# Performance work log

Hardware: AMD Instinct MI355X
Metric: run time of the kernel (lower is better)

The kernel has to match this reference:

```python
import jax, jax.numpy as jnp
import numpy as np

B, S, D = 8, 2048, 256


def setup_inputs() -> dict:
    key = jax.random.key(0)
    ks = jax.random.split(key, 8)
    nodes = jax.random.normal(ks[0], (B, S, D), dtype=jnp.float32)
    mask = jax.random.randint(ks[1], (B, S), 0, 2, dtype=jnp.int32)
    # ensure at least one unmasked position per row to avoid all--inf softmax
    mask = mask.at[:, 0].set(1)
    scale = 1.0 / np.sqrt(D)
    Wq = jax.random.normal(ks[2], (D, D), dtype=jnp.float32) * scale
    bq = jnp.zeros((D,), dtype=jnp.float32)
    Wk = jax.random.normal(ks[3], (D, D), dtype=jnp.float32) * scale
    bk = jnp.zeros((D,), dtype=jnp.float32)
    Wv = jax.random.normal(ks[4], (D, D), dtype=jnp.float32) * scale
    bv = jnp.zeros((D,), dtype=jnp.float32)
    return {"nodes": nodes, "mask": mask, "Wq": Wq, "bq": bq,
            "Wk": Wk, "bk": bk, "Wv": Wv, "bv": bv}


def reference(nodes, mask, Wq, bq, Wk, bk, Wv, bv):
    # Linear layers: x @ W.T + b (torch nn.Linear convention)
    q = jnp.einsum('bsd,ed->bse', nodes, Wq) + bq   # [B,S,D]
    k = jnp.einsum('bsd,ed->bse', nodes, Wk) + bk
    v = jnp.einsum('bsd,ed->bse', nodes, Wv) + bv
    d = k.shape[-1]
    scores = jnp.einsum('bqd,bkd->bqk', q, k) / jnp.sqrt(jnp.float32(d))  # [B,S,S]
    # mask[b, j] == 0 masks key column j for every query row
    scores = jnp.where(mask[:, None, :] != 0, scores, -jnp.inf)
    attn = jax.nn.softmax(scores, axis=-1)           # [B,S,S]
    weighted = jnp.einsum('bqk,bkd->bqd', attn, v)   # [B,S,D]
    return jnp.mean(weighted, axis=1)                # [B,D]
```

## Files before the change

### kernel.cpp

```cpp
#include <hip/hip_runtime.h>
#include <hip/hip_bf16.h>
#include <stdint.h>


typedef short short8 __attribute__((ext_vector_type(8)));
typedef float floatx4 __attribute__((ext_vector_type(4)));
typedef float floatx2 __attribute__((ext_vector_type(2)));

#define MFMA16(a, b, c) __builtin_amdgcn_mfma_f32_16x16x32_bf16((a), (b), (c), 0, 0, 0)

#define ASYNC16(gsrc, ldst)                                                    \
    __builtin_amdgcn_global_load_lds(                                          \
        (__attribute__((address_space(1))) void*)(void*)(gsrc),                \
        (__attribute__((address_space(3))) void*)(ldst), 16, 0, 0)

static __device__ __forceinline__ unsigned short f2bf(float f) {
    union { float f; unsigned u; } v; v.f = f;
    unsigned r = v.u + 0x7fffu + ((v.u >> 16) & 1u);
    return (unsigned short)(r >> 16);
}
static __device__ __forceinline__ float bf2f(unsigned short h) {
    union { unsigned u; float f; } v; v.u = ((unsigned)h) << 16;
    return v.f;
}

__global__ __launch_bounds__(256) void k_cc(
    const float* __restrict__ nodes, const float* __restrict__ Wq,
    const float* __restrict__ Wk, const float* __restrict__ Wv,
    unsigned short* __restrict__ nbf, unsigned short* __restrict__ wbf,
    const int* __restrict__ mask, int* __restrict__ cidx, int* __restrict__ cnt,
    float* __restrict__ zbase ,
    float* __restrict__ outp )
{
    int blk = blockIdx.x;
    if (blk < 2144) {
        int unit = blk * 256 + threadIdx.x;
        const float* src;
        unsigned short* dst;
        int off;
        if (unit < 524288) {
            src = nodes; dst = nbf; off = unit * 8;
        } else {
            int j = (unit - 524288) * 8;
            int m = j >> 16;
            int r = j & 65535;
            src = (m == 0) ? Wq : (m == 1 ? Wk : Wv);
            dst = wbf + m * 65536;
            off = r;
        }
        float4 a = *(const float4*)(src + off);
        float4 b = *(const float4*)(src + off + 4);
        short8 o;
        o[0] = f2bf(a.x); o[1] = f2bf(a.y); o[2] = f2bf(a.z); o[3] = f2bf(a.w);
        o[4] = f2bf(b.x); o[5] = f2bf(b.y); o[6] = f2bf(b.z); o[7] = f2bf(b.w);
        *(short8*)(dst + off) = o;
        return;
    }
    if (blk < 2152) {
        if (threadIdx.x < 64) {
            int b = blk - 2144, lane = threadIdx.x;
            int base = 0;
            for (int c = 0; c < 2048; c += 64) {
                int m = mask[b * 2048 + c + lane];
                unsigned long long bal = __ballot(m != 0);
                int pre = __popcll(bal & ((1ull << lane) - 1ull));
                if (m) cidx[b * 2048 + base + pre] = c + lane;
                base += __popcll(bal);
            }
            if (lane == 0) cnt[b] = base;
            for (int i = base + lane; i < 2048; i += 64) cidx[b * 2048 + i] = 0;
        }
        return;
    }
    int idx = (blk - 2152) * 256 + threadIdx.x;
    float4 z = {0.f, 0.f, 0.f, 0.f};
#pragma unroll
    for (int j = 0; j < 2; ++j) {
        int p = idx + j * 4352;
        if (p < 8192) ((float4*)zbase)[p] = z;
        else ((float4*)outp)[p - 8192] = z;
    }
}

__global__ __launch_bounds__(256) void k_proj2a(
    const unsigned short* __restrict__ nbf,
    const unsigned short* __restrict__ wbf,
    const float* __restrict__ bq, const float* __restrict__ bk,
    const float* __restrict__ bv,
    unsigned short* __restrict__ qb, unsigned short* __restrict__ kb,
    unsigned short* __restrict__ vb)
{
    __shared__ __align__(16) unsigned short As[128 * 64];
    __shared__ __align__(16) unsigned short Bs[128 * 64];
    int tid = threadIdx.x, lane = tid & 63, wave = tid >> 6;
    int wm = wave & 1, wn = wave >> 1;
    int l15 = lane & 15, quad = lane >> 4;
    int mBase = blockIdx.x * 128;
    int nBase = blockIdx.y * 128;
    int z = blockIdx.z;
    const unsigned short* W = wbf + z * 65536;

    floatx4 acc[4][4] = {};

    for (int kc = 0; kc < 256; kc += 64) {
#pragma unroll
        for (int i = 0; i < 4; ++i) {
            int p = i * 256 + wave * 64 + lane;
            int row = p >> 3;
            int col8 = (p & 7) ^ (row & 7);
            int goff = row * 256 + kc + col8 * 8;
            unsigned short* dstA = &As[(i * 256 + wave * 64) * 8];
            unsigned short* dstB = &Bs[(i * 256 + wave * 64) * 8];
            ASYNC16(nbf + mBase * 256 + goff, dstA);
            ASYNC16(W + nBase * 256 + goff, dstB);
        }
        __syncthreads();
#pragma unroll
        for (int ks = 0; ks < 2; ++ks) {
            int c8 = ks * 4 + quad;
            short8 af[4], bfr[4];
#pragma unroll
            for (int i = 0; i < 4; ++i) {
                int row = wm * 64 + i * 16 + l15;
                af[i] = *(const short8*)(&As[(row * 8 + (c8 ^ (row & 7))) * 8]);
            }
#pragma unroll
            for (int i = 0; i < 4; ++i) {
                int row = wn * 64 + i * 16 + l15;
                bfr[i] = *(const short8*)(&Bs[(row * 8 + (c8 ^ (row & 7))) * 8]);
            }
#pragma unroll
            for (int mi = 0; mi < 4; ++mi)
#pragma unroll
                for (int ni = 0; ni < 4; ++ni)
                    acc[mi][ni] = MFMA16(af[mi], bfr[ni], acc[mi][ni]);
        }
        __syncthreads();
    }

    const float* bias = (z == 0) ? bq : (z == 1 ? bk : bv);
    unsigned short* out = (z == 0) ? qb : (z == 1 ? kb : vb);
    float scale = (z == 0) ? 0.0625f : 1.0f;
#pragma unroll
    for (int mi = 0; mi < 4; ++mi)
#pragma unroll
        for (int ni = 0; ni < 4; ++ni) {
            int col = nBase + wn * 64 + ni * 16 + l15;
            float bval = bias[col];
#pragma unroll
            for (int r = 0; r < 4; ++r) {
                int row = mBase + wm * 64 + mi * 16 + quad * 4 + r;
                out[row * 256 + col] = f2bf((acc[mi][ni][r] + bval) * scale);
            }
        }
}

__global__ __launch_bounds__(256) void k_repack(
    const unsigned short* __restrict__ kb, const int* __restrict__ cidx,
    const int* __restrict__ cnt_g, unsigned short* __restrict__ kbt)
{
    int c = blockIdx.x, b = blockIdx.y;
    int cnt = cnt_g[b];
    if (c * 64 >= cnt) return;
    size_t obase = ((size_t)b * 32 + c) * 16384;
#pragma unroll
    for (int i = 0; i < 8; ++i) {
        int idx = i * 256 + threadIdx.x;
        int du = idx >> 6, key = idx & 63;
        int krow = cidx[b * 2048 + c * 64 + key];
        short8 v = *(const short8*)(kb + ((size_t)b * 2048 + krow) * 256 + du * 8);
        *(short8*)(kbt + obase + (size_t)idx * 8) = v;
    }
}

__global__ __launch_bounds__(256) void k_pass1v(
    const unsigned short* __restrict__ qb, const unsigned short* __restrict__ kbt,
    const int* __restrict__ cnt_g, float* __restrict__ lsum_g,
    unsigned char* __restrict__ pbuf)
{
    __shared__ __align__(16) unsigned short kt[16384];
    int tid = threadIdx.x, lane = tid & 63, wave = tid >> 6;
    int l15 = lane & 15, quad = lane >> 4;
    int b = blockIdx.z;
    int cnt = cnt_g[b];
    int nchunk = (cnt + 63) >> 6;
    int qBase = blockIdx.x * 128 + wave * 32;
    int qcg = blockIdx.x * 4 + wave;

    short8 qf[2][8];
#pragma unroll
    for (int mi = 0; mi < 2; ++mi)
#pragma unroll
        for (int ks = 0; ks < 8; ++ks)
            qf[mi][ks] = *(const short8*)(qb + (b * 2048 + qBase + mi * 16 + l15) * 256 + ks * 32 + quad * 8);

    float ls[2][4] = {};
    for (int c = blockIdx.y; c < nchunk; c += 4) {
        const unsigned short* src = kbt + ((size_t)b * 32 + c) * 16384;
#pragma unroll
        for (int i = 0; i < 8; ++i) {
            int seg = wave * 8 + i;
            ASYNC16(src + seg * 512 + lane * 8, &kt[seg * 512]);
        }
        __syncthreads();
#pragma unroll
        for (int nt = 0; nt < 4; ++nt) {
            short8 kf[8];
#pragma unroll
            for (int ks = 0; ks < 8; ++ks)
                kf[ks] = *(const short8*)(&kt[((ks * 4 + quad) * 64 + nt * 16 + l15) * 8]);
            floatx4 acc[2] = {};
#pragma unroll
            for (int ks = 0; ks < 8; ++ks) {
                acc[0] = MFMA16(qf[0][ks], kf[ks], acc[0]);
                acc[1] = MFMA16(qf[1][ks], kf[ks], acc[1]);
            }
            float bias = (c * 64 + nt * 16 + l15 < cnt) ? 0.0f : -1e30f;
            float e[2][4];
#pragma unroll
            for (int mi = 0; mi < 2; ++mi)
#pragma unroll
                for (int r = 0; r < 4; ++r) {
                    e[mi][r] = __expf(acc[mi][r] + bias);
                    ls[mi][r] += e[mi][r];
                }
            int ktile = c * 4 + nt;
            if (ktile < 96) {
                int w0 = __builtin_amdgcn_cvt_pk_fp8_f32(e[0][0], e[0][1], 0, 0);
                w0 = __builtin_amdgcn_cvt_pk_fp8_f32(e[0][2], e[0][3], w0, 1);
                int w1 = __builtin_amdgcn_cvt_pk_fp8_f32(e[1][0], e[1][1], 0, 0);
                w1 = __builtin_amdgcn_cvt_pk_fp8_f32(e[1][2], e[1][3], w1, 1);
                size_t off = ((((size_t)b * 96 + ktile) * 64 + qcg) * 64 + lane) * 8;
                uint2 pv; pv.x = (unsigned)w0; pv.y = (unsigned)w1;
                *(uint2*)(pbuf + off) = pv;
            }
        }
        __syncthreads();
    }
#pragma unroll
    for (int mi = 0; mi < 2; ++mi)
#pragma unroll
        for (int r = 0; r < 4; ++r) {
            float v = ls[mi][r];
            v += __shfl_xor(v, 1); v += __shfl_xor(v, 2);
            v += __shfl_xor(v, 4); v += __shfl_xor(v, 8);
            if (l15 == 0)
                atomicAdd(&lsum_g[b * 2048 + qBase + mi * 16 + quad * 4 + r], v);
        }
}

__global__ __launch_bounds__(512) void k_wred5(
    const unsigned char* __restrict__ pbuf, const float* __restrict__ lsum_g,
    const int* __restrict__ cidx, const int* __restrict__ cnt_g,
    float* __restrict__ wsum_g)
{
    __shared__ float linv_p[2048];
    int tid = threadIdx.x, lane = tid & 63, wave = tid >> 6;
    int l15 = lane & 15, quad = lane >> 4;
    int b = blockIdx.z;
    int ktile = blockIdx.y * 8 + wave;

#pragma unroll
    for (int i = 0; i < 4; ++i) {
        int idx = i * 512 + tid;
        int qcg = idx >> 5, qd = (idx >> 3) & 3, j = idx & 7;
        int q = qcg * 32 + (j >> 2) * 16 + qd * 4 + (j & 3);
        linv_p[idx] = 1.0f / lsum_g[b * 2048 + q];
    }
    __syncthreads();

    int cnt = cnt_g[b];
    if (ktile >= 96 || ktile * 16 >= cnt) return;

    int qcg0 = blockIdx.x * 32;
    float acc = 0.f;
#pragma unroll 4
    for (int qcg = qcg0; qcg < qcg0 + 32; ++qcg) {
        size_t off = ((((size_t)b * 96 + ktile) * 64 + qcg) * 64 + lane) * 8;
        uint2 pv = *(const uint2*)(pbuf + off);
        const float* lv = &linv_p[(qcg * 4 + quad) * 8];
        floatx2 p01 = __builtin_amdgcn_cvt_pk_f32_fp8(pv.x, 0);
        floatx2 p23 = __builtin_amdgcn_cvt_pk_f32_fp8(pv.x, 1);
        floatx2 p45 = __builtin_amdgcn_cvt_pk_f32_fp8(pv.y, 0);
        floatx2 p67 = __builtin_amdgcn_cvt_pk_f32_fp8(pv.y, 1);
        acc += p01[0] * lv[0] + p01[1] * lv[1] + p23[0] * lv[2] + p23[1] * lv[3]
             + p45[0] * lv[4] + p45[1] * lv[5] + p67[0] * lv[6] + p67[1] * lv[7];
    }
    acc += __shfl_xor(acc, 16);
    acc += __shfl_xor(acc, 32);
    int slot = ktile * 16 + l15;
    if (lane < 16 && slot < cnt)
        atomicAdd(&wsum_g[b * 2048 + cidx[b * 2048 + slot]], acc);
}

__global__ __launch_bounds__(256) void k_out(
    const float* __restrict__ wsum_g, const unsigned short* __restrict__ vb,
    float* __restrict__ outp)
{
    int b = blockIdx.y;
    int d = threadIdx.x;
    int k0 = blockIdx.x * 128;
    float acc = 0.f;
#pragma unroll 4
    for (int k = k0; k < k0 + 128; ++k) {
        float wv = wsum_g[b * 2048 + k];
        acc += wv * bf2f(vb[(b * 2048 + k) * 256 + d]);
    }
    atomicAdd(&outp[b * 256 + d], acc * (1.0f / 2048.0f));
}

extern "C" void kernel_launch(void* const* d_in, const int* in_sizes, int n_in,
                              void* d_out, int out_size, void* d_ws, size_t ws_size,
                              hipStream_t stream)
{
    const float* nodes = (const float*)d_in[0];
    const int*   mask  = (const int*)d_in[1];
    const float* Wq    = (const float*)d_in[2];
    const float* bq    = (const float*)d_in[3];
    const float* Wk    = (const float*)d_in[4];
    const float* bk    = (const float*)d_in[5];
    const float* Wv    = (const float*)d_in[6];
    const float* bv    = (const float*)d_in[7];
    float* out = (float*)d_out;

    unsigned short* qb  = (unsigned short*)d_ws;
    unsigned short* kb  = qb + 4194304;
    unsigned short* vb  = kb + 4194304;
    float* lsum = (float*)(vb + 4194304);
    float* wsum = lsum + 16384;
    int*   cnt  = (int*)(wsum + 16384);
    int*   cidx = cnt + 16;
    unsigned short* kbt = (unsigned short*)(cidx + 16384);
    unsigned short* X   = kbt + 4194304;
    unsigned short* nbf = X;
    unsigned short* wbf = X + 4194304;
    unsigned char* pbuf = (unsigned char*)X;

    k_cc<<<2169, 256, 0, stream>>>(nodes, Wq, Wk, Wv, nbf, wbf,
                                   mask, cidx, cnt, lsum, out);
    k_proj2a<<<dim3(128, 2, 3), 256, 0, stream>>>(nbf, wbf, bq, bk, bv, qb, kb, vb);
    k_repack<<<dim3(32, 8), 256, 0, stream>>>(kb, cidx, cnt, kbt);
    k_pass1v<<<dim3(16, 4, 8), 256, 0, stream>>>(qb, kbt, cnt, lsum, pbuf);
    k_wred5<<<dim3(2, 16, 8), 512, 0, stream>>>(pbuf, lsum, cidx, cnt, wsum);
    k_out<<<dim3(16, 8), 256, 0, stream>>>(wsum, vb, out);
}
```

Baseline: 142.3 us.

## Fuse K repack into projection epilogue via slot map scatter

The mask-compaction step now also builds a per-row slot map and zero-fills the padded tail of the compacted K buffer. The projection kernel writes K directly into the compacted, transposed kbt layout using that map, so the separate repack kernel and the intermediate K buffer are removed. This saves one launch and a full read/write pass over K. In exchange, the K epilogue does scattered 2-byte stores with a per-row slot lookup, which may coalesce poorly.

```diff
diff --git a/kernel.cpp b/kernel.cpp
--- a/kernel.cpp
+++ b/kernel.cpp
@@ -29,6 +29,8 @@
     const float* __restrict__ Wk, const float* __restrict__ Wv,
     unsigned short* __restrict__ nbf, unsigned short* __restrict__ wbf,
     const int* __restrict__ mask, int* __restrict__ cidx, int* __restrict__ cnt,
+    int* __restrict__ slot_of ,
+    unsigned short* __restrict__ kbt,
     float* __restrict__ zbase ,
     float* __restrict__ outp )
 {
@@ -64,11 +66,26 @@
                 int m = mask[b * 2048 + c + lane];
                 unsigned long long bal = __ballot(m != 0);
                 int pre = __popcll(bal & ((1ull << lane) - 1ull));
-                if (m) cidx[b * 2048 + base + pre] = c + lane;
+                if (m) {
+                    cidx[b * 2048 + base + pre] = c + lane;
+                    slot_of[b * 2048 + c + lane] = base + pre;
+                } else {
+                    slot_of[b * 2048 + c + lane] = -1;
+                }
                 base += __popcll(bal);
             }
             if (lane == 0) cnt[b] = base;
             for (int i = base + lane; i < 2048; i += 64) cidx[b * 2048 + i] = 0;
+            int cntPad = (base + 63) & ~63;
+            int pad = cntPad - base;
+            short8 z8 = {};
+            for (int i = lane; i < pad * 32; i += 64) {
+                int slot = base + (i >> 5);
+                int du = i & 31;
+                size_t off = ((size_t)b * 32 + (slot >> 6)) * 16384
+                           + ((size_t)du * 64 + (slot & 63)) * 8;
+                *(short8*)(kbt + off) = z8;
+            }
         }
         return;
     }
@@ -82,12 +99,13 @@
     }
 }
 
-__global__ __launch_bounds__(256) void k_proj2a(
+__global__ __launch_bounds__(256) void k_proj2b(
     const unsigned short* __restrict__ nbf,
     const unsigned short* __restrict__ wbf,
     const float* __restrict__ bq, const float* __restrict__ bk,
     const float* __restrict__ bv,
-    unsigned short* __restrict__ qb, unsigned short* __restrict__ kb,
+    const int* __restrict__ slot_of,
+    unsigned short* __restrict__ qb, unsigned short* __restrict__ kbt,
     unsigned short* __restrict__ vb)
 {
     __shared__ __align__(16) unsigned short As[128 * 64];
@@ -139,37 +157,41 @@
     }
 
     const float* bias = (z == 0) ? bq : (z == 1 ? bk : bv);
-    unsigned short* out = (z == 0) ? qb : (z == 1 ? kb : vb);
     float scale = (z == 0) ? 0.0625f : 1.0f;
-#pragma unroll
-    for (int mi = 0; mi < 4; ++mi)
-#pragma unroll
-        for (int ni = 0; ni < 4; ++ni) {
-            int col = nBase + wn * 64 + ni * 16 + l15;
-            float bval = bias[col];
-#pragma unroll
-            for (int r = 0; r < 4; ++r) {
-                int row = mBase + wm * 64 + mi * 16 + quad * 4 + r;
-                out[row * 256 + col] = f2bf((acc[mi][ni][r] + bval) * scale);
-            }
-        }
-}
-
-__global__ __launch_bounds__(256) void k_repack(
-    const unsigned short* __restrict__ kb, const int* __restrict__ cidx,
-    const int* __restrict__ cnt_g, unsigned short* __restrict__ kbt)
-{
-    int c = blockIdx.x, b = blockIdx.y;
-    int cnt = cnt_g[b];
-    if (c * 64 >= cnt) return;
-    size_t obase = ((size_t)b * 32 + c) * 16384;
-#pragma unroll
-    for (int i = 0; i < 8; ++i) {
-        int idx = i * 256 + threadIdx.x;
-        int du = idx >> 6, key = idx & 63;
-        int krow = cidx[b * 2048 + c * 64 + key];
-        short8 v = *(const short8*)(kb + ((size_t)b * 2048 + krow) * 256 + du * 8);
-        *(short8*)(kbt + obase + (size_t)idx * 8) = v;
+    if (z == 1) {
+#pragma unroll
+        for (int mi = 0; mi < 4; ++mi)
+#pragma unroll
+            for (int ni = 0; ni < 4; ++ni) {
+                int col = nBase + wn * 64 + ni * 16 + l15;
+                float bval = bias[col];
+                int du = col >> 3, cj = col & 7;
+#pragma unroll
+                for (int r = 0; r < 4; ++r) {
+                    int row = mBase + wm * 64 + mi * 16 + quad * 4 + r;
+                    int slot = slot_of[row];
+                    if (slot >= 0) {
+                        int b = row >> 11;
+                        size_t off = ((size_t)b * 32 + (slot >> 6)) * 16384
+                                   + ((size_t)du * 64 + (slot & 63)) * 8 + cj;
+                        kbt[off] = f2bf(acc[mi][ni][r] + bval);
+                    }
+                }
+            }
+    } else {
+        unsigned short* out = (z == 0) ? qb : vb;
+#pragma unroll
+        for (int mi = 0; mi < 4; ++mi)
+#pragma unroll
+            for (int ni = 0; ni < 4; ++ni) {
+                int col = nBase + wn * 64 + ni * 16 + l15;
+                float bval = bias[col];
+#pragma unroll
+                for (int r = 0; r < 4; ++r) {
+                    int row = mBase + wm * 64 + mi * 16 + quad * 4 + r;
+                    out[row * 256 + col] = f2bf((acc[mi][ni][r] + bval) * scale);
+                }
+            }
     }
 }
 
@@ -324,22 +346,22 @@
     float* out = (float*)d_out;
 
     unsigned short* qb  = (unsigned short*)d_ws;
-    unsigned short* kb  = qb + 4194304;
-    unsigned short* vb  = kb + 4194304;
+    unsigned short* vb  = qb + 4194304;
     float* lsum = (float*)(vb + 4194304);
     float* wsum = lsum + 16384;
     int*   cnt  = (int*)(wsum + 16384);
     int*   cidx = cnt + 16;
-    unsigned short* kbt = (unsigned short*)(cidx + 16384);
+    int*   slot_of = cidx + 16384;
+    unsigned short* kbt = (unsigned short*)(slot_of + 16384);
     unsigned short* X   = kbt + 4194304;
     unsigned short* nbf = X;
     unsigned short* wbf = X + 4194304;
     unsigned char* pbuf = (unsigned char*)X;
 
     k_cc<<<2169, 256, 0, stream>>>(nodes, Wq, Wk, Wv, nbf, wbf,
-                                   mask, cidx, cnt, lsum, out);
-    k_proj2a<<<dim3(128, 2, 3), 256, 0, stream>>>(nbf, wbf, bq, bk, bv, qb, kb, vb);
-    k_repack<<<dim3(32, 8), 256, 0, stream>>>(kb, cidx, cnt, kbt);
+                                   mask, cidx, cnt, slot_of, kbt, lsum, out);
+    k_proj2b<<<dim3(128, 2, 3), 256, 0, stream>>>(nbf, wbf, bq, bk, bv,
+                                                  slot_of, qb, kbt, vb);
     k_pass1v<<<dim3(16, 4, 8), 256, 0, stream>>>(qb, kbt, cnt, lsum, pbuf);
     k_wred5<<<dim3(2, 16, 8), 512, 0, stream>>>(pbuf, lsum, cidx, cnt, wsum);
     k_out<<<dim3(16, 8), 256, 0, stream>>>(wsum, vb, out);
```

Result: no change. 140.8 us (median of 2 runs) (-1.0%).
